# Kernel optimization log

Hardware: AMD Instinct MI355X
Metric: run time of the kernel (lower is better)

Reference implementation:

```python
import jax, jax.numpy as jnp
import numpy as np

B, CIN, COUT, H, W, K = 4, 128, 128, 128, 128, 3
KK = K * K


def setup_inputs() -> dict:
    key = jax.random.key(0)
    ks = jax.random.split(key, 6)
    return {
        "inp": jax.random.normal(ks[0], (B, CIN, H, W), jnp.float32),
        "feat": jax.random.normal(ks[1], (B, CIN, H, W), jnp.float32),
        # small offset-conv weights keep predicted offsets in a realistic few-pixel range
        "w_off": jax.random.normal(ks[2], (3 * KK, CIN, K, K), jnp.float32) * 0.01,
        "b_off": jnp.zeros((3 * KK,), jnp.float32),
        "w_dc": jax.random.normal(ks[3], (COUT, CIN, K, K), jnp.float32) * (1.0 / np.sqrt(CIN * KK)),
        "b_dc": jnp.zeros((COUT,), jnp.float32),
    }


def _conv3x3(x, w, b):
    # stride=1, padding=1, dilation=1, groups=1 (module defaults)
    y = jax.lax.conv_general_dilated(x, w, (1, 1), ((1, 1), (1, 1)),
                                     dimension_numbers=("NCHW", "OIHW", "NCHW"))
    return y + b[None, :, None, None]


def _modulated_deform_conv(x, offset, mask, w, b):
    # DCNv2: offset [B, 2*KK, H, W] interleaved (y, x) per kernel tap, mask [B, KK, H, W]
    b_, c, h, wd = x.shape
    ky = jnp.repeat(jnp.arange(K), K)  # kernel row index per tap, [KK]
    kx = jnp.tile(jnp.arange(K), K)    # kernel col index per tap, [KK]
    off = offset.reshape(b_, KK, 2, h, wd)
    # sampling positions: out_idx - pad + k*dilation + learned offset
    py = off[:, :, 0] + (jnp.arange(h)[None, None, :, None] + ky[None, :, None, None] - 1).astype(offset.dtype)
    px = off[:, :, 1] + (jnp.arange(wd)[None, None, None, :] + kx[None, :, None, None] - 1).astype(offset.dtype)
    y0 = jnp.floor(py)
    x0 = jnp.floor(px)
    ly = py - y0  # bilinear fractions (grad flows to offsets through these)
    lx = px - x0
    y0i = y0.astype(jnp.int32)
    x0i = x0.astype(jnp.int32)
    x_flat = x.reshape(b_, c, h * wd)

    def corner(yi, xi, wgt):
        valid = (yi >= 0) & (yi < h) & (xi >= 0) & (xi < wd)  # zero padding outside
        idx = jnp.clip(yi, 0, h - 1) * wd + jnp.clip(xi, 0, wd - 1)
        g = jnp.take_along_axis(x_flat, idx.reshape(b_, 1, -1), axis=2).reshape(b_, c, KK, h, wd)
        return g * (wgt * valid)[:, None]

    val = (corner(y0i,     x0i,     (1 - ly) * (1 - lx))
         + corner(y0i,     x0i + 1, (1 - ly) * lx)
         + corner(y0i + 1, x0i,     ly * (1 - lx))
         + corner(y0i + 1, x0i + 1, ly * lx))
    val = val * mask[:, None]  # modulation
    out = jnp.einsum("bckhw,ock->bohw", val, w.reshape(w.shape[0], c, KK))
    return out + b[None, :, None, None]


def reference(inp, feat, w_off, b_off, w_dc, b_dc):
    o = _conv3x3(feat, w_off, b_off)
    o1, o2, m = jnp.split(o, 3, axis=1)
    offset = jnp.concatenate([o1, o2], axis=1)
    mask = jax.nn.sigmoid(m)
    return _modulated_deform_conv(inp, offset, mask, w_dc, b_dc)
```

## Files before the change

### kernel.cpp

```cpp
#include <hip/hip_runtime.h>
#include <math.h>

#define B_    4
#define CIN_  128
#define COUT_ 128
#define H_    128
#define W_    128
#define HW_   (H_*W_)
#define KK_   9

typedef __attribute__((ext_vector_type(8))) short short8;
typedef __attribute__((ext_vector_type(4))) float f32x4;
typedef _Float16 h8 __attribute__((ext_vector_type(8)));
typedef float f2v __attribute__((ext_vector_type(2), aligned(4)));

static __device__ __forceinline__ unsigned f2bf(float f) {
    union { float f; unsigned u; } v; v.f = f;
    return (v.u + 0x7fffu + ((v.u >> 16) & 1u)) >> 16;
}
static __device__ __forceinline__ unsigned short f2h(float f) {
    union { _Float16 h; unsigned short u; } v; v.h = (_Float16)f;
    return v.u;
}


__global__ __launch_bounds__(256) void prep_kernel(
    const float* __restrict__ inp, const float* __restrict__ w_dc,
    const float* __restrict__ w_off, unsigned short* __restrict__ inpT,
    unsigned short* __restrict__ w_swz, unsigned short* __restrict__ woff_swz)
{
    const int bx = blockIdx.x;
    const int tid = threadIdx.x;
    __shared__ unsigned short s_T[128 * 142];

    if (bx < 512) {
        const int b = bx >> 7, y = bx & 127;
        const float* src = inp + (size_t)b * CIN_ * HW_ + y * W_;
        const int xs = (tid & 63) * 2;
        const int c0 = tid >> 6;
#pragma unroll 4
        for (int p = 0; p < 32; ++p) {
            int c = c0 + 4 * p;
            f2v d = *(const f2v*)(src + (size_t)c * HW_ + xs);
            s_T[xs * 142 + c]       = f2h(d.x);
            s_T[(xs + 1) * 142 + c] = f2h(d.y);
        }
        __syncthreads();
        unsigned short* dst = inpT + (size_t)bx * (W_ * CIN_);
        const int cs = (tid & 15) * 8;
        const int x0 = tid >> 4;
#pragma unroll
        for (int p = 0; p < 8; ++p) {
            int x = x0 + 16 * p;
            unsigned r[4];
#pragma unroll
            for (int j = 0; j < 4; ++j) {
                unsigned lo = s_T[x * 142 + cs + 2 * j];
                unsigned hi = s_T[x * 142 + cs + 2 * j + 1];
                r[j] = lo | (hi << 16);
            }
            *(int4*)(dst + (size_t)x * CIN_ + cs) = make_int4(r[0], r[1], r[2], r[3]);
        }
    } else if (bx < 584) {
        int idx = (bx - 512) * 256 + tid;
        int q   = idx >> 9;
        int rem = idx & 511;
        int ocb = rem >> 6;
        int l   = rem & 63;
        int cbq = q / 9;
        int k   = q - cbq * 9;
        int cb  = (cbq << 5) + ((l >> 4) << 3);
        int oc  = (ocb << 4) + (l & 15);
        unsigned r[4];
#pragma unroll
        for (int j = 0; j < 4; ++j) {
            float f0 = w_dc[((size_t)(oc * CIN_ + cb + 2 * j    )) * KK_ + k];
            float f1 = w_dc[((size_t)(oc * CIN_ + cb + 2 * j + 1)) * KK_ + k];
            r[j] = (unsigned)f2h(f0) | ((unsigned)f2h(f1) << 16);
        }
        *(int4*)&w_swz[(size_t)idx * 8] = make_int4(r[0], r[1], r[2], r[3]);
    } else {
        int idx = (bx - 584) * 256 + tid;
        int q   = idx >> 7;
        int rem = idx & 127;
        int l   = rem & 63;
        int cbq = q / 9;
        int k   = q - cbq * 9;
        int cb  = (cbq << 5) + ((l >> 4) << 3);
        int oc  = ((rem >> 6) << 4) + (l & 15);
        unsigned r[4];
#pragma unroll
        for (int j = 0; j < 4; ++j) {
            float f0 = 0.f, f1 = 0.f;
            if (oc < 27) {
                f0 = w_off[((size_t)(oc * CIN_ + cb + 2 * j    )) * KK_ + k];
                f1 = w_off[((size_t)(oc * CIN_ + cb + 2 * j + 1)) * KK_ + k];
            }
            r[j] = f2bf(f0) | (f2bf(f1) << 16);
        }
        *(int4*)&woff_swz[(size_t)idx * 8] = make_int4(r[0], r[1], r[2], r[3]);
    }
}

__global__ __launch_bounds__(256, 4) void fused_kernel(
    const float* __restrict__ feat, const unsigned short* __restrict__ inpT,
    const unsigned short* __restrict__ woff_swz, const unsigned short* __restrict__ w_swz,
    const float* __restrict__ b_off, const float* __restrict__ b_dc,
    float* __restrict__ out)
{
    const int tid = threadIdx.x;
    const int bx = blockIdx.x;
    const int lidx = ((bx & 7) << 7) | (bx >> 3);
    const int b  = lidx >> 8;
    const int h  = (lidx & 255) >> 1;
    const int w0 = (lidx & 1) << 6;

    __shared__ __align__(16) unsigned short s_R0[7936];
    __shared__ float  offv[27][65];
    __shared__ int2   s_midx[576];
    __shared__ float4 s_mwgt[576];

    unsigned short (*s_F)[66][40] = (unsigned short (*)[66][40])s_R0;
    unsigned short (*s_V)[64][40] = (unsigned short (*)[64][40])s_R0;

    const int lane = tid & 63;
    const int wave = tid >> 6;
    const int kg = lane >> 4, pn = lane & 15;

    {
        const float* fbase = feat + (size_t)b * CIN_ * HW_;
        f32x4 acc[2];
        acc[0] = (f32x4){0.f, 0.f, 0.f, 0.f};
        acc[1] = (f32x4){0.f, 0.f, 0.f, 0.f};

        for (int cb = 0; cb < 4; ++cb) {
            if (cb) __syncthreads();

#pragma unroll
            for (int r = 0; r < 3; ++r) {
                const int y = h + r - 1;
                const bool yv = (unsigned)y < (unsigned)H_;
                const float* rowp = fbase + (size_t)(cb << 5) * HW_ + y * W_;
#pragma unroll
                for (int j = 0; j < 4; ++j) {
                    int item = tid + (j << 8);
                    int c = item >> 5;
                    int e = item & 31;
                    int x0 = w0 - 1 + 2 * e;
                    int hx = min(max(x0, 0), W_ - 2);
                    float v0 = 0.f, v1 = 0.f;
                    if (yv) {
                        f2v p = *(const f2v*)(rowp + (size_t)c * HW_ + hx);
                        v0 = (x0 == hx) ? p.x : ((x0 < hx) ? 0.f : p.y);
                        v1 = (x0 == hx) ? p.y : ((x0 < hx) ? p.x : 0.f);
                    }
                    s_F[r][2 * e    ][c] = (unsigned short)f2bf(v0);
                    s_F[r][2 * e + 1][c] = (unsigned short)f2bf(v1);
                }
                if (tid < 32) {
                    int c = tid;
                    int x0 = w0 + 63;
                    int hx = min(x0, W_ - 2);
                    float v0 = 0.f, v1 = 0.f;
                    if (yv) {
                        f2v p = *(const f2v*)(rowp + (size_t)c * HW_ + hx);
                        v0 = (x0 == hx) ? p.x : p.y;
                        v1 = (x0 == hx) ? p.y : 0.f;
                    }
                    s_F[r][64][c] = (unsigned short)f2bf(v0);
                    s_F[r][65][c] = (unsigned short)f2bf(v1);
                }
            }
            __syncthreads();

            const int qb2 = cb * 18;
            const short8* wb = (const short8*)woff_swz;
            short8 a0 = wb[(size_t)(qb2    ) * 64 + lane];
            short8 a1 = wb[(size_t)(qb2 + 1) * 64 + lane];
#pragma unroll
            for (int k = 0; k < 9; ++k) {
                const int ky = k / 3, kx = k - 3 * ky;
                short8 bfr = *(const short8*)&s_F[ky][wave * 16 + pn + kx][kg * 8];
                short8 na0, na1;
                if (k < 8) {
                    na0 = wb[(size_t)(qb2 + 2 * k + 2) * 64 + lane];
                    na1 = wb[(size_t)(qb2 + 2 * k + 3) * 64 + lane];
                }
                acc[0] = __builtin_amdgcn_mfma_f32_16x16x32_bf16(a0, bfr, acc[0], 0, 0, 0);
                acc[1] = __builtin_amdgcn_mfma_f32_16x16x32_bf16(a1, bfr, acc[1], 0, 0, 0);
                if (k < 8) { a0 = na0; a1 = na1; }
            }
        }

        const int row0 = (lane >> 4) << 2;
        const int col  = lane & 15;
        const int pwl  = wave * 16 + col;
#pragma unroll
        for (int mt = 0; mt < 2; ++mt) {
#pragma unroll
            for (int i = 0; i < 4; ++i) {
                int oc = mt * 16 + row0 + i;
                if (oc < 27) {
                    float v = acc[mt][i] + b_off[oc];
                    if (oc >= 18) v = 1.f / (1.f + __expf(-v));
                    offv[oc][pwl] = v;
                }
            }
        }
    }
    __syncthreads();

    for (int i = tid; i < 576; i += 256) {
        int k = i >> 6, p = i & 63;
        int ky = k / 3, kx = k - ky * 3;
        int pw = w0 + p;
        float offy = offv[2 * k    ][p];
        float offx = offv[2 * k + 1][p];
        float mask = offv[18 + k   ][p];
        float py  = offy + (float)(h  + ky - 1);
        float px_ = offx + (float)(pw + kx - 1);
        float y0f = floorf(py), x0f = floorf(px_);
        float ly = py - y0f, lx = px_ - x0f;
        int y0 = (int)y0f, x0 = (int)x0f;
        int y1 = y0 + 1;
        int hx = min(max(x0, 0), W_ - 2);
        float wlo = 0.f, whi = 0.f;
        if (x0 == hx)          { wlo = 1.f - lx; whi = lx; }
        else if (x0 == hx - 1) { wlo = lx; }
        else if (x0 == hx + 1) { whi = 1.f - lx; }
        float wt_top = ((unsigned)y0 < (unsigned)H_) ? (1.f - ly) * mask : 0.f;
        float wt_bot = ((unsigned)y1 < (unsigned)H_) ? ly * mask : 0.f;
        int cy0 = min(max(y0, 0), H_ - 1), cy1 = min(max(y1, 0), H_ - 1);
        s_midx[i] = make_int2(cy0 * W_ + hx, cy1 * W_ + hx);
        s_mwgt[i] = make_float4(wt_top * wlo, wt_top * whi,
                                wt_bot * wlo, wt_bot * whi);
    }
    __syncthreads();

    const int px = tid >> 2;
    const int cs = tid & 3;
    const char* inpTb = (const char*)(inpT + (size_t)b * CIN_ * HW_);

    f32x4 acc2[2][4];
#pragma unroll
    for (int mt = 0; mt < 2; ++mt)
#pragma unroll
        for (int nt = 0; nt < 4; ++nt) acc2[mt][nt] = (f32x4){0.f, 0.f, 0.f, 0.f};

    h8 pf0, pf1, pf2, pf3;

    auto issue = [&](int qq) {
        int cbq = qq / 9;
        int k   = qq - cbq * 9;
        int2 id = s_midx[(k << 6) + px];
        int coff = (cbq << 6) + (cs << 4);
        const char* g0 = inpTb + ((size_t)(unsigned)id.x << 8) + coff;
        const char* g1 = inpTb + ((size_t)(unsigned)id.y << 8) + coff;
        pf0 = *(const h8*)(g0);
        pf1 = *(const h8*)(g0 + 256);
        pf2 = *(const h8*)(g1);
        pf3 = *(const h8*)(g1 + 256);
    };

    issue(0);

    for (int q = 0; q < 36; ++q) {
        int k = q - (q / 9) * 9;

        float4 wt = s_mwgt[(k << 6) + px];
        h8 v = pf0 * (_Float16)wt.x;
        v += pf1 * (_Float16)wt.y;
        v += pf2 * (_Float16)wt.z;
        v += pf3 * (_Float16)wt.w;

        const h8* wp = (const h8*)w_swz + (size_t)(q * 8 + wave * 2) * 64 + lane;
        h8 af0 = wp[0];
        h8 af1 = wp[64];

        *(h8*)&s_V[q & 1][px][cs << 3] = v;

        int qn = (q + 1 < 36) ? q + 1 : 35;
        issue(qn);

        __syncthreads();

#pragma unroll
        for (int nt = 0; nt < 4; ++nt) {
            h8 bfr = *(const h8*)&s_V[q & 1][nt * 16 + pn][kg * 8];
            acc2[0][nt] = __builtin_amdgcn_mfma_f32_16x16x32_f16(af0, bfr, acc2[0][nt], 0, 0, 0);
            acc2[1][nt] = __builtin_amdgcn_mfma_f32_16x16x32_f16(af1, bfr, acc2[1][nt], 0, 0, 0);
        }
    }

    const int row0 = (lane >> 4) << 2;
    const int col  = lane & 15;
#pragma unroll
    for (int mt = 0; mt < 2; ++mt) {
#pragma unroll
        for (int nt = 0; nt < 4; ++nt) {
            int pw = w0 + nt * 16 + col;
#pragma unroll
            for (int i = 0; i < 4; ++i) {
                int oc = wave * 32 + mt * 16 + row0 + i;
                out[((size_t)(b * COUT_ + oc)) * HW_ + h * W_ + pw] =
                    acc2[mt][nt][i] + b_dc[oc];
            }
        }
    }
}

extern "C" void kernel_launch(void* const* d_in, const int* in_sizes, int n_in,
                              void* d_out, int out_size, void* d_ws, size_t ws_size,
                              hipStream_t stream)
{
    const float* inp   = (const float*)d_in[0];
    const float* feat  = (const float*)d_in[1];
    const float* w_off = (const float*)d_in[2];
    const float* b_off = (const float*)d_in[3];
    const float* w_dc  = (const float*)d_in[4];
    const float* b_dc  = (const float*)d_in[5];
    float* out  = (float*)d_out;
    unsigned short* w_swz    = (unsigned short*)d_ws;
    unsigned short* woff_swz = (unsigned short*)((char*)d_ws + 294912);
    unsigned short* inpT     = (unsigned short*)((char*)d_ws + 368640);

    prep_kernel<<<dim3(602), dim3(256), 0, stream>>>(inp, w_dc, w_off, inpT, w_swz, woff_swz);
    fused_kernel<<<dim3(1024), dim3(256), 0, stream>>>(feat, inpT, woff_swz, w_swz, b_off, b_dc, out);
}
```

Baseline: 171.3 us.

## Pre-transpose feat to channel-last fp16 and prefetch deform weights across barrier

The prep kernel now also transposes feat into a channel-last fp16 buffer, so the offset-conv stage loads 16-byte vectors straight into shared memory instead of strided fp32 loads with per-element bf16 conversion. The offset conv switches from bf16 to fp16 MFMA, and its weights are converted to fp16 to match. In the main loop, the deform-conv weight fragments are prefetched one iteration ahead, and __syncthreads is replaced by an explicit lgkmcnt wait plus s_barrier. This adds an extra full transpose pass over feat in the prep kernel and more workspace, and fp16 offsets may lose range compared with bf16.

```diff
diff --git a/kernel.cpp b/kernel.cpp
--- a/kernel.cpp
+++ b/kernel.cpp
@@ -14,10 +14,6 @@
 typedef _Float16 h8 __attribute__((ext_vector_type(8)));
 typedef float f2v __attribute__((ext_vector_type(2), aligned(4)));
 
-static __device__ __forceinline__ unsigned f2bf(float f) {
-    union { float f; unsigned u; } v; v.f = f;
-    return (v.u + 0x7fffu + ((v.u >> 16) & 1u)) >> 16;
-}
 static __device__ __forceinline__ unsigned short f2h(float f) {
     union { _Float16 h; unsigned short u; } v; v.h = (_Float16)f;
     return v.u;
@@ -25,17 +21,20 @@
 
 
 __global__ __launch_bounds__(256) void prep_kernel(
-    const float* __restrict__ inp, const float* __restrict__ w_dc,
-    const float* __restrict__ w_off, unsigned short* __restrict__ inpT,
+    const float* __restrict__ inp, const float* __restrict__ feat,
+    const float* __restrict__ w_dc, const float* __restrict__ w_off,
+    unsigned short* __restrict__ inpT, unsigned short* __restrict__ featT,
     unsigned short* __restrict__ w_swz, unsigned short* __restrict__ woff_swz)
 {
     const int bx = blockIdx.x;
     const int tid = threadIdx.x;
     __shared__ unsigned short s_T[128 * 142];
 
-    if (bx < 512) {
-        const int b = bx >> 7, y = bx & 127;
-        const float* src = inp + (size_t)b * CIN_ * HW_ + y * W_;
+    if (bx < 1024) {
+        const int bi = bx & 511;
+        const int b = bi >> 7, y = bi & 127;
+        const float* src = (bx < 512 ? inp : feat) + (size_t)b * CIN_ * HW_ + y * W_;
+        unsigned short* dstb = (bx < 512 ? inpT : featT) + (size_t)bi * (W_ * CIN_);
         const int xs = (tid & 63) * 2;
         const int c0 = tid >> 6;
 #pragma unroll 4
@@ -46,7 +45,6 @@
             s_T[(xs + 1) * 142 + c] = f2h(d.y);
         }
         __syncthreads();
-        unsigned short* dst = inpT + (size_t)bx * (W_ * CIN_);
         const int cs = (tid & 15) * 8;
         const int x0 = tid >> 4;
 #pragma unroll
@@ -59,10 +57,10 @@
                 unsigned hi = s_T[x * 142 + cs + 2 * j + 1];
                 r[j] = lo | (hi << 16);
             }
-            *(int4*)(dst + (size_t)x * CIN_ + cs) = make_int4(r[0], r[1], r[2], r[3]);
-        }
-    } else if (bx < 584) {
-        int idx = (bx - 512) * 256 + tid;
+            *(int4*)(dstb + (size_t)x * CIN_ + cs) = make_int4(r[0], r[1], r[2], r[3]);
+        }
+    } else if (bx < 1096) {
+        int idx = (bx - 1024) * 256 + tid;
         int q   = idx >> 9;
         int rem = idx & 511;
         int ocb = rem >> 6;
@@ -80,7 +78,7 @@
         }
         *(int4*)&w_swz[(size_t)idx * 8] = make_int4(r[0], r[1], r[2], r[3]);
     } else {
-        int idx = (bx - 584) * 256 + tid;
+        int idx = (bx - 1096) * 256 + tid;
         int q   = idx >> 7;
         int rem = idx & 127;
         int l   = rem & 63;
@@ -96,14 +94,14 @@
                 f0 = w_off[((size_t)(oc * CIN_ + cb + 2 * j    )) * KK_ + k];
                 f1 = w_off[((size_t)(oc * CIN_ + cb + 2 * j + 1)) * KK_ + k];
             }
-            r[j] = f2bf(f0) | (f2bf(f1) << 16);
+            r[j] = (unsigned)f2h(f0) | ((unsigned)f2h(f1) << 16);
         }
         *(int4*)&woff_swz[(size_t)idx * 8] = make_int4(r[0], r[1], r[2], r[3]);
     }
 }
 
 __global__ __launch_bounds__(256, 4) void fused_kernel(
-    const float* __restrict__ feat, const unsigned short* __restrict__ inpT,
+    const unsigned short* __restrict__ featT, const unsigned short* __restrict__ inpT,
     const unsigned short* __restrict__ woff_swz, const unsigned short* __restrict__ w_swz,
     const float* __restrict__ b_off, const float* __restrict__ b_dc,
     float* __restrict__ out)
@@ -128,66 +126,54 @@
     const int kg = lane >> 4, pn = lane & 15;
 
     {
-        const float* fbase = feat + (size_t)b * CIN_ * HW_;
+        const unsigned short* fT = featT;
         f32x4 acc[2];
         acc[0] = (f32x4){0.f, 0.f, 0.f, 0.f};
         acc[1] = (f32x4){0.f, 0.f, 0.f, 0.f};
 
+        const int me = tid >> 2;
+        const int mg = tid & 3;
+
         for (int cb = 0; cb < 4; ++cb) {
             if (cb) __syncthreads();
 
 #pragma unroll
             for (int r = 0; r < 3; ++r) {
-                const int y = h + r - 1;
-                const bool yv = (unsigned)y < (unsigned)H_;
-                const float* rowp = fbase + (size_t)(cb << 5) * HW_ + y * W_;
-#pragma unroll
-                for (int j = 0; j < 4; ++j) {
-                    int item = tid + (j << 8);
-                    int c = item >> 5;
-                    int e = item & 31;
-                    int x0 = w0 - 1 + 2 * e;
-                    int hx = min(max(x0, 0), W_ - 2);
-                    float v0 = 0.f, v1 = 0.f;
-                    if (yv) {
-                        f2v p = *(const f2v*)(rowp + (size_t)c * HW_ + hx);
-                        v0 = (x0 == hx) ? p.x : ((x0 < hx) ? 0.f : p.y);
-                        v1 = (x0 == hx) ? p.y : ((x0 < hx) ? p.x : 0.f);
-                    }
-                    s_F[r][2 * e    ][c] = (unsigned short)f2bf(v0);
-                    s_F[r][2 * e + 1][c] = (unsigned short)f2bf(v1);
-                }
-                if (tid < 32) {
-                    int c = tid;
-                    int x0 = w0 + 63;
-                    int hx = min(x0, W_ - 2);
-                    float v0 = 0.f, v1 = 0.f;
-                    if (yv) {
-                        f2v p = *(const f2v*)(rowp + (size_t)c * HW_ + hx);
-                        v0 = (x0 == hx) ? p.x : p.y;
-                        v1 = (x0 == hx) ? p.y : 0.f;
-                    }
-                    s_F[r][64][c] = (unsigned short)f2bf(v0);
-                    s_F[r][65][c] = (unsigned short)f2bf(v1);
-                }
+                int y = h + r - 1;
+                h8 d{};
+                if ((unsigned)y < (unsigned)H_)
+                    d = *(const h8*)(fT + (((size_t)(b * H_ + y) * W_ + (w0 + me)) * CIN_
+                                           + (cb << 5) + (mg << 3)));
+                *(h8*)&s_F[r][me + 1][mg << 3] = d;
+            }
+            if (tid < 24) {
+                int r = tid >> 3, side = (tid >> 2) & 1, g = tid & 3;
+                int x = side ? (w0 + 64) : (w0 - 1);
+                int t = side ? 65 : 0;
+                int y = h + r - 1;
+                h8 d{};
+                if (((unsigned)y < (unsigned)H_) & ((unsigned)x < (unsigned)W_))
+                    d = *(const h8*)(fT + (((size_t)(b * H_ + y) * W_ + x) * CIN_
+                                           + (cb << 5) + (g << 3)));
+                *(h8*)&s_F[r][t][g << 3] = d;
             }
             __syncthreads();
 
             const int qb2 = cb * 18;
-            const short8* wb = (const short8*)woff_swz;
-            short8 a0 = wb[(size_t)(qb2    ) * 64 + lane];
-            short8 a1 = wb[(size_t)(qb2 + 1) * 64 + lane];
+            const h8* wb = (const h8*)woff_swz;
+            h8 a0 = wb[(size_t)(qb2    ) * 64 + lane];
+            h8 a1 = wb[(size_t)(qb2 + 1) * 64 + lane];
 #pragma unroll
             for (int k = 0; k < 9; ++k) {
                 const int ky = k / 3, kx = k - 3 * ky;
-                short8 bfr = *(const short8*)&s_F[ky][wave * 16 + pn + kx][kg * 8];
-                short8 na0, na1;
+                h8 bfr = *(const h8*)&s_F[ky][wave * 16 + pn + kx][kg * 8];
+                h8 na0, na1;
                 if (k < 8) {
                     na0 = wb[(size_t)(qb2 + 2 * k + 2) * 64 + lane];
                     na1 = wb[(size_t)(qb2 + 2 * k + 3) * 64 + lane];
                 }
-                acc[0] = __builtin_amdgcn_mfma_f32_16x16x32_bf16(a0, bfr, acc[0], 0, 0, 0);
-                acc[1] = __builtin_amdgcn_mfma_f32_16x16x32_bf16(a1, bfr, acc[1], 0, 0, 0);
+                acc[0] = __builtin_amdgcn_mfma_f32_16x16x32_f16(a0, bfr, acc[0], 0, 0, 0);
+                acc[1] = __builtin_amdgcn_mfma_f32_16x16x32_f16(a1, bfr, acc[1], 0, 0, 0);
                 if (k < 8) { a0 = na0; a1 = na1; }
             }
         }
@@ -263,6 +249,9 @@
     };
 
     issue(0);
+    const h8* wp0 = (const h8*)w_swz + (size_t)(wave * 2) * 64 + lane;
+    h8 af0 = wp0[0];
+    h8 af1 = wp0[64];
 
     for (int q = 0; q < 36; ++q) {
         int k = q - (q / 9) * 9;
@@ -273,16 +262,17 @@
         v += pf2 * (_Float16)wt.z;
         v += pf3 * (_Float16)wt.w;
 
-        const h8* wp = (const h8*)w_swz + (size_t)(q * 8 + wave * 2) * 64 + lane;
-        h8 af0 = wp[0];
-        h8 af1 = wp[64];
-
         *(h8*)&s_V[q & 1][px][cs << 3] = v;
 
         int qn = (q + 1 < 36) ? q + 1 : 35;
         issue(qn);
-
-        __syncthreads();
+        const h8* wpn = (const h8*)w_swz + (size_t)(qn * 8 + wave * 2) * 64 + lane;
+        h8 na0 = wpn[0];
+        h8 na1 = wpn[64];
+
+        asm volatile("s_waitcnt lgkmcnt(0)" ::: "memory");
+        __builtin_amdgcn_s_barrier();
+        __builtin_amdgcn_sched_barrier(0);
 
 #pragma unroll
         for (int nt = 0; nt < 4; ++nt) {
@@ -290,6 +280,7 @@
             acc2[0][nt] = __builtin_amdgcn_mfma_f32_16x16x32_f16(af0, bfr, acc2[0][nt], 0, 0, 0);
             acc2[1][nt] = __builtin_amdgcn_mfma_f32_16x16x32_f16(af1, bfr, acc2[1][nt], 0, 0, 0);
         }
+        af0 = na0; af1 = na1;
     }
 
     const int row0 = (lane >> 4) << 2;
@@ -323,7 +314,10 @@
     unsigned short* w_swz    = (unsigned short*)d_ws;
     unsigned short* woff_swz = (unsigned short*)((char*)d_ws + 294912);
     unsigned short* inpT     = (unsigned short*)((char*)d_ws + 368640);
-
-    prep_kernel<<<dim3(602), dim3(256), 0, stream>>>(inp, w_dc, w_off, inpT, w_swz, woff_swz);
-    fused_kernel<<<dim3(1024), dim3(256), 0, stream>>>(feat, inpT, woff_swz, w_swz, b_off, b_dc, out);
+    unsigned short* featT    = (unsigned short*)((char*)d_ws + 368640 + 16777216);
+
+    prep_kernel<<<dim3(1114), dim3(256), 0, stream>>>(inp, feat, w_dc, w_off,
+                                                      inpT, featT, w_swz, woff_swz);
+    fused_kernel<<<dim3(1024), dim3(256), 0, stream>>>(featT, inpT, woff_swz, w_swz,
+                                                       b_off, b_dc, out);
 }
```

After: 163.8 us. -4.4%, faster.
